# Kernel optimization log

Hardware: AMD Instinct MI355X
Metric: run time of the kernel (lower is better)

Reference implementation:

```python
import jax, jax.numpy as jnp
import numpy as np

D_MODEL = 512
D_STATE = 16
EXPAND = 2
DT_RANK = 8
D_INNER = EXPAND * D_MODEL  # 1024
LN_EPS = 1e-5


def setup_inputs() -> dict:
    key = jax.random.key(0)
    ks = jax.random.split(key, 10)
    B, H, W = 8, 48, 48
    inp = {
        "x": jax.random.normal(ks[0], (B, H, W, D_MODEL), jnp.float32),
        # Linear weights stored [in, out] (torch weight transposed)
        "W_in": jax.random.normal(ks[1], (D_MODEL, 2 * D_INNER), jnp.float32) * 0.02,
        # depthwise conv kernel, HWIO with feature_group_count = D_INNER
        "conv_k": jax.random.normal(ks[2], (3, 3, 1, D_INNER), jnp.float32) * 0.1,
        "W_xproj": jax.random.normal(ks[3], (D_INNER, DT_RANK + 2 * D_STATE), jnp.float32) * 0.02,
        "W_dt": jax.random.uniform(ks[4], (DT_RANK, D_INNER), jnp.float32, -0.1, 0.1),
        "b_dt": jnp.full((D_INNER,), 0.1, jnp.float32),
        "A_log": jax.random.normal(ks[5], (D_STATE,), jnp.float32) * 0.02,
        "Dskip": jnp.ones((D_INNER,), jnp.float32),
        "W_dtN": jax.random.normal(ks[6], (D_INNER, D_STATE), jnp.float32) * 0.02,
        "b_dtN": jnp.zeros((D_STATE,), jnp.float32),
        "ln_g": jnp.ones((D_INNER,), jnp.float32),
        "ln_b": jnp.zeros((D_INNER,), jnp.float32),
        "W_out": jax.random.normal(ks[7], (D_INNER, D_MODEL), jnp.float32) * 0.02,
        "b_out": jnp.zeros((D_MODEL,), jnp.float32),
    }
    return inp


def _ss2d(x, W_in, conv_k, W_xproj, W_dt, b_dt, A_log, Dskip, W_dtN, b_dtN,
          ln_g, ln_b, W_out, b_out):
    B, H, W_, _ = x.shape
    L = H * W_
    # in_proj and split into x / gate z
    xz = x @ W_in                                   # [B,H,W,2*D_INNER]
    xh, z = jnp.split(xz, 2, axis=-1)
    # depthwise 3x3 conv (NHWC)
    xc = jax.lax.conv_general_dilated(
        xh, conv_k, window_strides=(1, 1), padding='SAME',
        dimension_numbers=('NHWC', 'HWIO', 'NHWC'),
        feature_group_count=D_INNER)                 # [B,H,W,D_INNER]
    # x_proj -> (dt_rank, B, C)
    xp = xc @ W_xproj
    dt_r = xp[..., :DT_RANK]
    Bp = xp[..., DT_RANK:DT_RANK + D_STATE]
    Cp = xp[..., DT_RANK + D_STATE:]
    dt = dt_r @ W_dt + b_dt                          # [B,H,W,D_INNER]
    # flatten spatial dims into sequence
    x_seq = xc.reshape(B, L, D_INNER)
    dt_seq = jax.nn.softplus(dt.reshape(B, L, D_INNER))
    B_seq = Bp.reshape(B, L, D_STATE)
    C_seq = Cp.reshape(B, L, D_STATE)
    A = -jnp.exp(A_log)                              # [N]; A_log expanded over D is constant per-row
    dtN = dt_seq @ W_dtN + b_dtN                     # dt_to_N_proj(softplus(dt)) -> [B,L,N]

    def step(h, t):
        x_t, dt_t, dtN_t, B_t, C_t = t               # [B,D],[B,D],[B,N],[B,N],[B,N]
        dA = jnp.exp(dt_t[:, :, None] * A)           # [B,D,N]
        dB = dtN_t * B_t                             # [B,N]
        h = dA * h + dB[:, None, :] * x_t[:, :, None]  # [B,D,N]
        y = jnp.einsum('bdn,bn->bd', h, C_t) + Dskip * x_t
        return h, y

    h0 = jnp.zeros((B, D_INNER, D_STATE), x.dtype)
    xs = (x_seq.transpose(1, 0, 2), dt_seq.transpose(1, 0, 2),
          dtN.transpose(1, 0, 2), B_seq.transpose(1, 0, 2),
          C_seq.transpose(1, 0, 2))
    _, ys = jax.lax.scan(step, h0, xs)               # ys: [L,B,D]
    y = ys.transpose(1, 0, 2).reshape(B, H, W_, D_INNER)
    # LayerNorm over channel dim
    mu = y.mean(-1, keepdims=True)
    var = ((y - mu) ** 2).mean(-1, keepdims=True)
    y = (y - mu) / jnp.sqrt(var + LN_EPS) * ln_g + ln_b
    # gate and out projection (dropout = identity in eval)
    y = y * jax.nn.silu(z)
    return y @ W_out + b_out


def reference(x, W_in, conv_k, W_xproj, W_dt, b_dt, A_log, Dskip, W_dtN,
              b_dtN, ln_g, ln_b, W_out, b_out):
    return _ss2d(x, W_in, conv_k, W_xproj, W_dt, b_dt, A_log, Dskip, W_dtN,
                 b_dtN, ln_g, ln_b, W_out, b_out)
```

## Files before the change

kernel.cpp:

```cpp
#include <hip/hip_runtime.h>
#include <hip/hip_bf16.h>

#define NBATCH 8
#define HEIGHT 48
#define WIDTH  48
#define DMODEL 512
#define DSTATE 16
#define DTRANK 8
#define DINNER 1024
#define LSEQ   (HEIGHT*WIDTH)
#define NROWS  (NBATCH*LSEQ)
#define NXP    40
#define NCH    32
#define TCH    72

typedef unsigned short u16;
typedef unsigned int   u32;
typedef __attribute__((ext_vector_type(8))) short short8;
typedef __attribute__((ext_vector_type(4))) float f32x4;

__device__ __forceinline__ float bf2f(u16 u) {
    u32 x = ((u32)u) << 16;
    return __uint_as_float(x);
}
__device__ __forceinline__ u16 f2bf(float f) {
    u32 x = __float_as_uint(f);
    u32 r = (x + 0x7FFFu + ((x >> 16) & 1u)) >> 16;
    return (u16)r;
}

#if __has_builtin(__builtin_amdgcn_exp2f)
__device__ __forceinline__ float EXP2(float x) { return __builtin_amdgcn_exp2f(x); }
#else
__device__ __forceinline__ float EXP2(float x) { return __expf(x * 0.69314718f); }
#endif

#define GLD16(g, l) __builtin_amdgcn_global_load_lds( \
    (const __attribute__((address_space(1))) void*)(g), \
    (__attribute__((address_space(3))) void*)(l), 16, 0, 0)

__global__ __launch_bounds__(256) void k_prep_x(const float* __restrict__ x,
                                                u16* __restrict__ xbf) {
    int i = blockIdx.x * 256 + threadIdx.x;
    float4 v = *reinterpret_cast<const float4*>(x + (size_t)i * 4);
    ushort4 o;
    o.x = f2bf(v.x); o.y = f2bf(v.y); o.z = f2bf(v.z); o.w = f2bf(v.w);
    *reinterpret_cast<ushort4*>(xbf + (size_t)i * 4) = o;
}

__global__ __launch_bounds__(256) void k_prep_w(const float* __restrict__ W_in,
                                                const float* __restrict__ W_out,
                                                const float* __restrict__ W_xproj,
                                                const float* __restrict__ W_dtN,
                                                u16* __restrict__ WinT,
                                                u16* __restrict__ WoutT,
                                                u16* __restrict__ WxpB,
                                                u16* __restrict__ WdtNB) {
    int idx = blockIdx.x * 256 + threadIdx.x;
    if (idx < 2048 * 512) {
        int n = idx >> 9, k = idx & 511;
        WinT[idx] = f2bf(W_in[(size_t)k * 2048 + n]);
    } else if (idx < 2048 * 512 + 512 * 1024) {
        int j = idx - 2048 * 512;
        int n = j >> 10, k = j & 1023;
        WoutT[j] = f2bf(W_out[(size_t)k * 512 + n]);
    } else if (idx < 2048 * 512 + 512 * 1024 + 48 * 1024) {
        int j = idx - (2048 * 512 + 512 * 1024);
        int n = j >> 10, k = j & 1023;
        WxpB[j] = (n < NXP) ? f2bf(W_xproj[(size_t)k * NXP + n]) : (u16)0;
    } else {
        int j = idx - (2048 * 512 + 512 * 1024 + 48 * 1024);
        int n = j >> 10, k = j & 1023;
        WdtNB[j] = f2bf(W_dtN[(size_t)k * DSTATE + n]);
    }
}

template<int K, int LDA, int LDB, int LDC, bool F32OUT>
__global__ __launch_bounds__(256) void k_gemm_mfma(const u16* __restrict__ A,
                                                   const u16* __restrict__ B,
                                                   const float* __restrict__ bias,
                                                   void* __restrict__ Cv) {
    __shared__ u16 As[128 * 32];
    __shared__ u16 Bs[128 * 32];
    const int tid = threadIdx.x;
    const int l   = tid & 63;
    const int w   = tid >> 6;
    const int wm  = w >> 1, wn = w & 1;
    const int m0  = blockIdx.y * 128, n0 = blockIdx.x * 128;
    const int srow = w * 32 + (l >> 2);
    const int sc   = l & 3;
    const int kh = l >> 4;
    const int lr = l & 15;

    f32x4 acc[4][4];
#pragma unroll
    for (int i = 0; i < 4; ++i)
#pragma unroll
        for (int j = 0; j < 4; ++j)
            acc[i][j] = (f32x4){0.f, 0.f, 0.f, 0.f};

    for (int k0 = 0; k0 < K; k0 += 32) {
#pragma unroll
        for (int i = 0; i < 2; ++i) {
            int r  = srow + i * 16;
            int cg = sc ^ ((r >> 1) & 3);
            const u16* ga = A + (size_t)(m0 + r) * LDA + k0 + cg * 8;
            const u16* gb = B + (size_t)(n0 + r) * LDB + k0 + cg * 8;
            GLD16(ga, As + (w * 2 + i) * 512);
            GLD16(gb, Bs + (w * 2 + i) * 512);
        }
        __syncthreads();
        short8 af[4], bfr[4];
#pragma unroll
        for (int f = 0; f < 4; ++f) {
            int ar = wm * 64 + f * 16 + lr;
            af[f]  = *reinterpret_cast<const short8*>(As + ar * 32 + ((kh ^ ((ar >> 1) & 3)) * 8));
            int br = wn * 64 + f * 16 + lr;
            bfr[f] = *reinterpret_cast<const short8*>(Bs + br * 32 + ((kh ^ ((br >> 1) & 3)) * 8));
        }
#pragma unroll
        for (int fm = 0; fm < 4; ++fm)
#pragma unroll
            for (int fn = 0; fn < 4; ++fn)
                acc[fm][fn] = __builtin_amdgcn_mfma_f32_16x16x32_bf16(
                    af[fm], bfr[fn], acc[fm][fn], 0, 0, 0);
        __syncthreads();
    }

#pragma unroll
    for (int fm = 0; fm < 4; ++fm) {
#pragma unroll
        for (int r = 0; r < 4; ++r) {
            int row = m0 + wm * 64 + fm * 16 + (l >> 4) * 4 + r;
#pragma unroll
            for (int fn = 0; fn < 4; ++fn) {
                int col = n0 + wn * 64 + fn * 16 + lr;
                if (F32OUT) {
                    ((float*)Cv)[(size_t)row * LDC + col] = acc[fm][fn][r] + bias[col];
                } else {
                    ((u16*)Cv)[(size_t)row * LDC + col] = f2bf(acc[fm][fn][r]);
                }
            }
        }
    }
}

__global__ __launch_bounds__(256) void k_conv(const u16* __restrict__ xz,
                                              const float* __restrict__ ck,
                                              u16* __restrict__ xc) {
    int row = blockIdx.x;
    int w = row % WIDTH;
    int hb = row / WIDTH;
    int h = hb % HEIGHT;
    int b = hb / HEIGHT;
    int c0 = threadIdx.x * 4;
    float a0 = 0.f, a1 = 0.f, a2 = 0.f, a3 = 0.f;
#pragma unroll
    for (int kh = 0; kh < 3; ++kh) {
        int hh = h + kh - 1;
        if (hh < 0 || hh >= HEIGHT) continue;
#pragma unroll
        for (int kw = 0; kw < 3; ++kw) {
            int ww = w + kw - 1;
            if (ww < 0 || ww >= WIDTH) continue;
            int r = (b * HEIGHT + hh) * WIDTH + ww;
            ushort4 v = *reinterpret_cast<const ushort4*>(xz + (size_t)r * 2048 + c0);
            float4 kv = *reinterpret_cast<const float4*>(ck + (kh * 3 + kw) * DINNER + c0);
            a0 = fmaf(bf2f(v.x), kv.x, a0);
            a1 = fmaf(bf2f(v.y), kv.y, a1);
            a2 = fmaf(bf2f(v.z), kv.z, a2);
            a3 = fmaf(bf2f(v.w), kv.w, a3);
        }
    }
    ushort4 ov;
    ov.x = f2bf(a0); ov.y = f2bf(a1); ov.z = f2bf(a2); ov.w = f2bf(a3);
    *reinterpret_cast<ushort4*>(xc + (size_t)row * DINNER + c0) = ov;
}

__global__ __launch_bounds__(256) void k_xproj(const u16* __restrict__ xc,
                                               const u16* __restrict__ WxpB,
                                               float* __restrict__ xp_out) {
    __shared__ u16 As[64 * 32];
    __shared__ u16 Bs[48 * 32];
    const int tid = threadIdx.x;
    const int l = tid & 63;
    const int w = tid >> 6;
    const int m0 = blockIdx.x * 64;
    const int kh = l >> 4, lr = l & 15;
    const int srow = w * 16 + (l >> 2);
    const int sc = l & 3;

    f32x4 acc[3];
    acc[0] = acc[1] = acc[2] = (f32x4){0.f, 0.f, 0.f, 0.f};

    for (int k0 = 0; k0 < 1024; k0 += 32) {
        {
            int cg = sc ^ ((srow >> 1) & 3);
            GLD16(xc + (size_t)(m0 + srow) * DINNER + k0 + cg * 8, As + w * 512);
            if (w < 3)
                GLD16(WxpB + (size_t)srow * 1024 + k0 + cg * 8, Bs + w * 512);
        }
        __syncthreads();
        int ar = w * 16 + lr;
        short8 af = *reinterpret_cast<const short8*>(As + ar * 32 + ((kh ^ ((ar >> 1) & 3)) * 8));
#pragma unroll
        for (int fn = 0; fn < 3; ++fn) {
            int br = fn * 16 + lr;
            short8 bf = *reinterpret_cast<const short8*>(Bs + br * 32 + ((kh ^ ((br >> 1) & 3)) * 8));
            acc[fn] = __builtin_amdgcn_mfma_f32_16x16x32_bf16(af, bf, acc[fn], 0, 0, 0);
        }
        __syncthreads();
    }
#pragma unroll
    for (int fn = 0; fn < 3; ++fn)
#pragma unroll
        for (int r = 0; r < 4; ++r) {
            int row = m0 + w * 16 + (l >> 4) * 4 + r;
            int col = fn * 16 + lr;
            if (col < NXP) xp_out[(size_t)row * NXP + col] = acc[fn][r];
        }
}

__global__ __launch_bounds__(256) void k_dt(const float* __restrict__ xp,
                                            const float* __restrict__ W_dt,
                                            const float* __restrict__ b_dt,
                                            u16* __restrict__ dt_out) {
    int gid = blockIdx.x * 256 + threadIdx.x;
    int row = gid >> 7;
    int dj  = (gid & 127) * 8;
    const float* xr = xp + (size_t)row * NXP;
    float4 xa = *reinterpret_cast<const float4*>(xr);
    float4 xb = *reinterpret_cast<const float4*>(xr + 4);
    float xv[8] = {xa.x, xa.y, xa.z, xa.w, xb.x, xb.y, xb.z, xb.w};
    float a[8];
    {
        float4 b0 = *reinterpret_cast<const float4*>(b_dt + dj);
        float4 b1 = *reinterpret_cast<const float4*>(b_dt + dj + 4);
        a[0]=b0.x; a[1]=b0.y; a[2]=b0.z; a[3]=b0.w;
        a[4]=b1.x; a[5]=b1.y; a[6]=b1.z; a[7]=b1.w;
    }
#pragma unroll
    for (int j = 0; j < 8; ++j) {
        float4 w0 = *reinterpret_cast<const float4*>(W_dt + j * DINNER + dj);
        float4 w1 = *reinterpret_cast<const float4*>(W_dt + j * DINNER + dj + 4);
        a[0] = fmaf(xv[j], w0.x, a[0]); a[1] = fmaf(xv[j], w0.y, a[1]);
        a[2] = fmaf(xv[j], w0.z, a[2]); a[3] = fmaf(xv[j], w0.w, a[3]);
        a[4] = fmaf(xv[j], w1.x, a[4]); a[5] = fmaf(xv[j], w1.y, a[5]);
        a[6] = fmaf(xv[j], w1.z, a[6]); a[7] = fmaf(xv[j], w1.w, a[7]);
    }
    short8 o;
#pragma unroll
    for (int j = 0; j < 8; ++j) {
        float dt = fmaxf(a[j], 0.f) + log1pf(__expf(-fabsf(a[j])));
        o[j] = (short)f2bf(dt);
    }
    *reinterpret_cast<short8*>(dt_out + (size_t)row * DINNER + dj) = o;
}

__global__ __launch_bounds__(256) void k_dtn(const u16* __restrict__ dtb,
                                             const u16* __restrict__ WdtNB,
                                             const float* __restrict__ b_dtN,
                                             const float* __restrict__ xp,
                                             float* __restrict__ dnBC) {
    __shared__ u16 As[64 * 32];
    __shared__ u16 Bs[16 * 32];
    const int tid = threadIdx.x;
    const int l = tid & 63;
    const int w = tid >> 6;
    const int m0 = blockIdx.x * 64;
    const int kh = l >> 4, lr = l & 15;
    const int srow = w * 16 + (l >> 2);
    const int sc = l & 3;

    f32x4 acc = (f32x4){0.f, 0.f, 0.f, 0.f};

    for (int k0 = 0; k0 < 1024; k0 += 32) {
        {
            int cg = sc ^ ((srow >> 1) & 3);
            GLD16(dtb + (size_t)(m0 + srow) * DINNER + k0 + cg * 8, As + w * 512);
            if (w == 0)
                GLD16(WdtNB + (size_t)srow * 1024 + k0 + cg * 8, Bs);
        }
        __syncthreads();
        int ar = w * 16 + lr;
        short8 af = *reinterpret_cast<const short8*>(As + ar * 32 + ((kh ^ ((ar >> 1) & 3)) * 8));
        short8 bf = *reinterpret_cast<const short8*>(Bs + lr * 32 + ((kh ^ ((lr >> 1) & 3)) * 8));
        acc = __builtin_amdgcn_mfma_f32_16x16x32_bf16(af, bf, acc, 0, 0, 0);
        __syncthreads();
    }
    float bn = b_dtN[lr];
#pragma unroll
    for (int r = 0; r < 4; ++r) {
        int row = m0 + w * 16 + (l >> 4) * 4 + r;
        float dn = acc[r] + bn;
        float Bv = xp[(size_t)row * NXP + DTRANK + lr];
        float Cv = xp[(size_t)row * NXP + DTRANK + DSTATE + lr];
        dnBC[(size_t)row * 32 + lr]      = dn * Bv;
        dnBC[(size_t)row * 32 + 16 + lr] = Cv;
    }
}

__global__ __launch_bounds__(256) void k_scan_p1(const u16* __restrict__ xc,
                                                 const u16* __restrict__ dtb,
                                                 const float* __restrict__ dnBC,
                                                 const float* __restrict__ A_log,
                                                 float* __restrict__ Pbuf,
                                                 float* __restrict__ Qbuf) {
    __shared__ float dnB_s[8][16];
    const int tid = threadIdx.x;
    const int blk = blockIdx.x;
    const int quarter = blk & 3;
    const int bc = blk >> 2;
    const int c = bc & (NCH - 1);
    const int b = bc >> 5;
    const int d = quarter * 256 + tid;

    float An2[16];
#pragma unroll
    for (int n = 0; n < 16; ++n)
        An2[n] = -__expf(A_log[n]) * 1.44269504f;

    float h[16];
#pragma unroll
    for (int n = 0; n < 16; ++n) h[n] = 0.f;
    float sdt = 0.f;

    const size_t row0 = (size_t)b * LSEQ + (size_t)c * TCH;
    for (int tt = 0; tt < TCH; tt += 8) {
        __syncthreads();
        if (tid < 128) {
            int t = tid >> 4, n = tid & 15;
            dnB_s[t][n] = dnBC[(row0 + tt + t) * 32 + n];
        }
        __syncthreads();
#pragma unroll
        for (int t = 0; t < 8; ++t) {
            size_t row = row0 + tt + t;
            float dt = bf2f(dtb[row * DINNER + d]);
            float xt = bf2f(xc[row * DINNER + d]);
            sdt += dt;
            const float4* dv = reinterpret_cast<const float4*>(&dnB_s[t][0]);
            float4 u0 = dv[0], u1 = dv[1], u2 = dv[2], u3 = dv[3];
            float u[16] = {u0.x,u0.y,u0.z,u0.w, u1.x,u1.y,u1.z,u1.w,
                           u2.x,u2.y,u2.z,u2.w, u3.x,u3.y,u3.z,u3.w};
#pragma unroll
            for (int n = 0; n < 16; ++n) {
                float dA = EXP2(dt * An2[n]);
                h[n] = fmaf(dA, h[n], u[n] * xt);
            }
        }
    }
    size_t base = ((size_t)bc << 14) + (size_t)d * 16;
#pragma unroll
    for (int n = 0; n < 16; ++n) {
        Pbuf[base + n] = EXP2(sdt * An2[n]);
        Qbuf[base + n] = h[n];
    }
}

__global__ __launch_bounds__(256) void k_scan_p2(const float* __restrict__ Pbuf,
                                                 float* __restrict__ Qbuf) {
    int tid = blockIdx.x * 256 + threadIdx.x;
    int b = tid >> 14, rem = tid & 16383;
    float h = 0.f;
    for (int c = 0; c < NCH; ++c) {
        size_t idx = ((size_t)(b * NCH + c) << 14) + rem;
        float P = Pbuf[idx];
        float q = Qbuf[idx];
        Qbuf[idx] = h;
        h = fmaf(P, h, q);
    }
}

__global__ __launch_bounds__(256) void k_scan_p3(const u16* __restrict__ xc,
                                                 const u16* __restrict__ dtb,
                                                 const float* __restrict__ dnBC,
                                                 const float* __restrict__ A_log,
                                                 const float* __restrict__ Dskip,
                                                 const float* __restrict__ Qbuf,
                                                 u16* __restrict__ ybuf) {
    __shared__ float S_s[8][32];
    const int tid = threadIdx.x;
    const int blk = blockIdx.x;
    const int quarter = blk & 3;
    const int bc = blk >> 2;
    const int c = bc & (NCH - 1);
    const int b = bc >> 5;
    const int d = quarter * 256 + tid;

    float An2[16];
#pragma unroll
    for (int n = 0; n < 16; ++n)
        An2[n] = -__expf(A_log[n]) * 1.44269504f;

    float h[16];
    size_t base = ((size_t)bc << 14) + (size_t)d * 16;
#pragma unroll
    for (int n = 0; n < 16; ++n) h[n] = Qbuf[base + n];
    float Dsk = Dskip[d];

    const size_t row0 = (size_t)b * LSEQ + (size_t)c * TCH;
    for (int tt = 0; tt < TCH; tt += 8) {
        __syncthreads();
        {
            int t = tid >> 5, j = tid & 31;
            S_s[t][j] = dnBC[(row0 + tt + t) * 32 + j];
        }
        __syncthreads();
#pragma unroll
        for (int t = 0; t < 8; ++t) {
            size_t row = row0 + tt + t;
            float dt = bf2f(dtb[row * DINNER + d]);
            float xt = bf2f(xc[row * DINNER + d]);
            const float4* sv = reinterpret_cast<const float4*>(&S_s[t][0]);
            float4 u0 = sv[0], u1 = sv[1], u2 = sv[2], u3 = sv[3];
            float4 c0 = sv[4], c1 = sv[5], c2 = sv[6], c3 = sv[7];
            float u[16]  = {u0.x,u0.y,u0.z,u0.w, u1.x,u1.y,u1.z,u1.w,
                            u2.x,u2.y,u2.z,u2.w, u3.x,u3.y,u3.z,u3.w};
            float cv[16] = {c0.x,c0.y,c0.z,c0.w, c1.x,c1.y,c1.z,c1.w,
                            c2.x,c2.y,c2.z,c2.w, c3.x,c3.y,c3.z,c3.w};
            float ys[4] = {Dsk * xt, 0.f, 0.f, 0.f};
#pragma unroll
            for (int n = 0; n < 16; ++n) {
                float dA = EXP2(dt * An2[n]);
                h[n] = fmaf(dA, h[n], u[n] * xt);
                ys[n & 3] = fmaf(h[n], cv[n], ys[n & 3]);
            }
            ybuf[row * 2048 + d] = f2bf((ys[0] + ys[1]) + (ys[2] + ys[3]));
        }
    }
}

__global__ __launch_bounds__(256) void k_ln_gate(u16* __restrict__ xz,
                                                 const float* __restrict__ ln_g,
                                                 const float* __restrict__ ln_b) {
    __shared__ float red[8];
    int row = blockIdx.x, tid = threadIdx.x;
    u16* yrow = xz + (size_t)row * 2048;
    int c0 = tid * 4;
    ushort4 v = *reinterpret_cast<const ushort4*>(yrow + c0);
    float y0 = bf2f(v.x), y1 = bf2f(v.y), y2 = bf2f(v.z), y3 = bf2f(v.w);
    float s = y0 + y1 + y2 + y3;
    float q = y0 * y0 + y1 * y1 + y2 * y2 + y3 * y3;
#pragma unroll
    for (int m = 32; m; m >>= 1) {
        s += __shfl_xor(s, m, 64);
        q += __shfl_xor(q, m, 64);
    }
    int lane = tid & 63, wv = tid >> 6;
    if (lane == 0) { red[wv] = s; red[4 + wv] = q; }
    __syncthreads();
    s = red[0] + red[1] + red[2] + red[3];
    q = red[4] + red[5] + red[6] + red[7];
    float mu = s * (1.f / DINNER);
    float var = q * (1.f / DINNER) - mu * mu;
    float rstd = rsqrtf(var + 1e-5f);
    ushort4 zv = *reinterpret_cast<const ushort4*>(yrow + DINNER + c0);
    float4 lg = *reinterpret_cast<const float4*>(ln_g + c0);
    float4 lb = *reinterpret_cast<const float4*>(ln_b + c0);
    float z0 = bf2f(zv.x), z1 = bf2f(zv.y), z2 = bf2f(zv.z), z3 = bf2f(zv.w);
    float g0 = ((y0 - mu) * rstd * lg.x + lb.x) * (z0 / (1.f + __expf(-z0)));
    float g1 = ((y1 - mu) * rstd * lg.y + lb.y) * (z1 / (1.f + __expf(-z1)));
    float g2 = ((y2 - mu) * rstd * lg.z + lb.z) * (z2 / (1.f + __expf(-z2)));
    float g3 = ((y3 - mu) * rstd * lg.w + lb.w) * (z3 / (1.f + __expf(-z3)));
    ushort4 ov;
    ov.x = f2bf(g0); ov.y = f2bf(g1); ov.z = f2bf(g2); ov.w = f2bf(g3);
    *reinterpret_cast<ushort4*>(yrow + c0) = ov;
}

extern "C" void kernel_launch(void* const* d_in, const int* in_sizes, int n_in,
                              void* d_out, int out_size, void* d_ws, size_t ws_size,
                              hipStream_t stream) {
    const float* x       = (const float*)d_in[0];
    const float* W_in    = (const float*)d_in[1];
    const float* conv_k  = (const float*)d_in[2];
    const float* W_xproj = (const float*)d_in[3];
    const float* W_dt    = (const float*)d_in[4];
    const float* b_dt    = (const float*)d_in[5];
    const float* A_log   = (const float*)d_in[6];
    const float* Dskip   = (const float*)d_in[7];
    const float* W_dtN   = (const float*)d_in[8];
    const float* b_dtN   = (const float*)d_in[9];
    const float* ln_g    = (const float*)d_in[10];
    const float* ln_b    = (const float*)d_in[11];
    const float* W_out   = (const float*)d_in[12];
    const float* b_out   = (const float*)d_in[13];
    float* out = (float*)d_out;

    char* ws = (char*)d_ws;
    size_t off = 0;
    u16*   xz    = (u16*)(ws + off); off += (size_t)NROWS * 2048 * 2;
    u16*   xc    = (u16*)(ws + off); off += (size_t)NROWS * 1024 * 2;
    u16*   dtb   = (u16*)(ws + off); off += (size_t)NROWS * 1024 * 2;
    float* xpb   = (float*)(ws + off); off += (size_t)NROWS * NXP * 4;
    float* dnBC  = (float*)(ws + off); off += (size_t)NROWS * 32 * 4;
    char*  scr   = ws + off; off += 2 * (size_t)NBATCH * NCH * DINNER * DSTATE * 4;
    u16*   xbf   = (u16*)scr;
    float* Pbuf  = (float*)scr;
    float* Qbuf  = (float*)(scr + (size_t)NBATCH * NCH * DINNER * DSTATE * 4);
    u16*   WinT  = (u16*)(ws + off); off += (size_t)2048 * 512 * 2;
    u16*   WoutT = (u16*)(ws + off); off += (size_t)512 * 1024 * 2;
    u16*   WxpB  = (u16*)(ws + off); off += (size_t)48 * 1024 * 2;
    u16*   WdtNB = (u16*)(ws + off); off += (size_t)16 * 1024 * 2;

    k_prep_x<<<(NROWS * DMODEL / 4) / 256, 256, 0, stream>>>(x, xbf);
    k_prep_w<<<(2048 * 512 + 512 * 1024 + 48 * 1024 + 16 * 1024) / 256, 256, 0, stream>>>(
        W_in, W_out, W_xproj, W_dtN, WinT, WoutT, WxpB, WdtNB);
    k_gemm_mfma<512, 512, 512, 2048, false>
        <<<dim3(2048 / 128, NROWS / 128), 256, 0, stream>>>(xbf, WinT, nullptr, xz);
    k_conv<<<NROWS, 256, 0, stream>>>(xz, conv_k, xc);
    k_xproj<<<NROWS / 64, 256, 0, stream>>>(xc, WxpB, xpb);
    k_dt<<<(NROWS * DINNER / 8) / 256, 256, 0, stream>>>(xpb, W_dt, b_dt, dtb);
    k_dtn<<<NROWS / 64, 256, 0, stream>>>(dtb, WdtNB, b_dtN, xpb, dnBC);
    k_scan_p1<<<NBATCH * NCH * 4, 256, 0, stream>>>(xc, dtb, dnBC, A_log,
                                                    Pbuf, Qbuf);
    k_scan_p2<<<(NBATCH * DINNER * DSTATE) / 256, 256, 0, stream>>>(Pbuf, Qbuf);
    k_scan_p3<<<NBATCH * NCH * 4, 256, 0, stream>>>(xc, dtb, dnBC, A_log,
                                                    Dskip, Qbuf, xz);
    k_ln_gate<<<NROWS, 256, 0, stream>>>(xz, ln_g, ln_b);
    k_gemm_mfma<1024, 2048, 1024, 512, true>
        <<<dim3(DMODEL / 128, NROWS / 128), 256, 0, stream>>>(xz, WoutT, b_out, out);
}
```

Before: 373.6 us.

## Drop LDS staging in scan kernels and transpose P/Q carry layout

The chunked-scan pass-1 and pass-3 kernels no longer stage dnB/C rows through shared memory behind barriers. Each thread now reads them straight from global memory as uniform float4 loads, which removes the __syncthreads pairs. The inter-chunk P/Q buffers switch from [d][n] to [n][d] layout, so per-state stores and loads become coalesced across threads. The cost is redundant scalar/vector global loads per wave that rely on cache hits.

```diff
diff --git a/kernel.cpp b/kernel.cpp
--- a/kernel.cpp
+++ b/kernel.cpp
@@ -306,7 +306,6 @@
                                                  const float* __restrict__ A_log,
                                                  float* __restrict__ Pbuf,
                                                  float* __restrict__ Qbuf) {
-    __shared__ float dnB_s[8][16];
     const int tid = threadIdx.x;
     const int blk = blockIdx.x;
     const int quarter = blk & 3;
@@ -326,35 +325,27 @@
     float sdt = 0.f;
 
     const size_t row0 = (size_t)b * LSEQ + (size_t)c * TCH;
-    for (int tt = 0; tt < TCH; tt += 8) {
-        __syncthreads();
-        if (tid < 128) {
-            int t = tid >> 4, n = tid & 15;
-            dnB_s[t][n] = dnBC[(row0 + tt + t) * 32 + n];
-        }
-        __syncthreads();
-#pragma unroll
-        for (int t = 0; t < 8; ++t) {
-            size_t row = row0 + tt + t;
-            float dt = bf2f(dtb[row * DINNER + d]);
-            float xt = bf2f(xc[row * DINNER + d]);
-            sdt += dt;
-            const float4* dv = reinterpret_cast<const float4*>(&dnB_s[t][0]);
-            float4 u0 = dv[0], u1 = dv[1], u2 = dv[2], u3 = dv[3];
-            float u[16] = {u0.x,u0.y,u0.z,u0.w, u1.x,u1.y,u1.z,u1.w,
-                           u2.x,u2.y,u2.z,u2.w, u3.x,u3.y,u3.z,u3.w};
-#pragma unroll
-            for (int n = 0; n < 16; ++n) {
-                float dA = EXP2(dt * An2[n]);
-                h[n] = fmaf(dA, h[n], u[n] * xt);
-            }
-        }
-    }
-    size_t base = ((size_t)bc << 14) + (size_t)d * 16;
+#pragma unroll 4
+    for (int t = 0; t < TCH; ++t) {
+        size_t row = row0 + t;
+        float dt = bf2f(dtb[row * DINNER + d]);
+        float xt = bf2f(xc[row * DINNER + d]);
+        const float4* dv = reinterpret_cast<const float4*>(dnBC + row * 32);
+        float4 u0 = dv[0], u1 = dv[1], u2 = dv[2], u3 = dv[3];
+        sdt += dt;
+        float u[16] = {u0.x,u0.y,u0.z,u0.w, u1.x,u1.y,u1.z,u1.w,
+                       u2.x,u2.y,u2.z,u2.w, u3.x,u3.y,u3.z,u3.w};
+#pragma unroll
+        for (int n = 0; n < 16; ++n) {
+            float dA = EXP2(dt * An2[n]);
+            h[n] = fmaf(dA, h[n], u[n] * xt);
+        }
+    }
+    size_t base = ((size_t)bc << 14) + d;
 #pragma unroll
     for (int n = 0; n < 16; ++n) {
-        Pbuf[base + n] = EXP2(sdt * An2[n]);
-        Qbuf[base + n] = h[n];
+        Pbuf[base + (size_t)n * DINNER] = EXP2(sdt * An2[n]);
+        Qbuf[base + (size_t)n * DINNER] = h[n];
     }
 }
 
@@ -379,7 +370,6 @@
                                                  const float* __restrict__ Dskip,
                                                  const float* __restrict__ Qbuf,
                                                  u16* __restrict__ ybuf) {
-    __shared__ float S_s[8][32];
     const int tid = threadIdx.x;
     const int blk = blockIdx.x;
     const int quarter = blk & 3;
@@ -394,40 +384,32 @@
         An2[n] = -__expf(A_log[n]) * 1.44269504f;
 
     float h[16];
-    size_t base = ((size_t)bc << 14) + (size_t)d * 16;
-#pragma unroll
-    for (int n = 0; n < 16; ++n) h[n] = Qbuf[base + n];
+    size_t base = ((size_t)bc << 14) + d;
+#pragma unroll
+    for (int n = 0; n < 16; ++n) h[n] = Qbuf[base + (size_t)n * DINNER];
     float Dsk = Dskip[d];
 
     const size_t row0 = (size_t)b * LSEQ + (size_t)c * TCH;
-    for (int tt = 0; tt < TCH; tt += 8) {
-        __syncthreads();
-        {
-            int t = tid >> 5, j = tid & 31;
-            S_s[t][j] = dnBC[(row0 + tt + t) * 32 + j];
-        }
-        __syncthreads();
-#pragma unroll
-        for (int t = 0; t < 8; ++t) {
-            size_t row = row0 + tt + t;
-            float dt = bf2f(dtb[row * DINNER + d]);
-            float xt = bf2f(xc[row * DINNER + d]);
-            const float4* sv = reinterpret_cast<const float4*>(&S_s[t][0]);
-            float4 u0 = sv[0], u1 = sv[1], u2 = sv[2], u3 = sv[3];
-            float4 c0 = sv[4], c1 = sv[5], c2 = sv[6], c3 = sv[7];
-            float u[16]  = {u0.x,u0.y,u0.z,u0.w, u1.x,u1.y,u1.z,u1.w,
-                            u2.x,u2.y,u2.z,u2.w, u3.x,u3.y,u3.z,u3.w};
-            float cv[16] = {c0.x,c0.y,c0.z,c0.w, c1.x,c1.y,c1.z,c1.w,
-                            c2.x,c2.y,c2.z,c2.w, c3.x,c3.y,c3.z,c3.w};
-            float ys[4] = {Dsk * xt, 0.f, 0.f, 0.f};
-#pragma unroll
-            for (int n = 0; n < 16; ++n) {
-                float dA = EXP2(dt * An2[n]);
-                h[n] = fmaf(dA, h[n], u[n] * xt);
-                ys[n & 3] = fmaf(h[n], cv[n], ys[n & 3]);
-            }
-            ybuf[row * 2048 + d] = f2bf((ys[0] + ys[1]) + (ys[2] + ys[3]));
-        }
+#pragma unroll 2
+    for (int t = 0; t < TCH; ++t) {
+        size_t row = row0 + t;
+        float dt = bf2f(dtb[row * DINNER + d]);
+        float xt = bf2f(xc[row * DINNER + d]);
+        const float4* sv = reinterpret_cast<const float4*>(dnBC + row * 32);
+        float4 u0 = sv[0], u1 = sv[1], u2 = sv[2], u3 = sv[3];
+        float4 c0 = sv[4], c1 = sv[5], c2 = sv[6], c3 = sv[7];
+        float u[16]  = {u0.x,u0.y,u0.z,u0.w, u1.x,u1.y,u1.z,u1.w,
+                        u2.x,u2.y,u2.z,u2.w, u3.x,u3.y,u3.z,u3.w};
+        float cv[16] = {c0.x,c0.y,c0.z,c0.w, c1.x,c1.y,c1.z,c1.w,
+                        c2.x,c2.y,c2.z,c2.w, c3.x,c3.y,c3.z,c3.w};
+        float ys[4] = {Dsk * xt, 0.f, 0.f, 0.f};
+#pragma unroll
+        for (int n = 0; n < 16; ++n) {
+            float dA = EXP2(dt * An2[n]);
+            h[n] = fmaf(dA, h[n], u[n] * xt);
+            ys[n & 3] = fmaf(h[n], cv[n], ys[n & 3]);
+        }
+        ybuf[row * 2048 + d] = f2bf((ys[0] + ys[1]) + (ys[2] + ys[3]));
     }
 }
 
```

New measurement: 363.1 us. 2.8% less time.
